# Optimization experiments

Hardware: AMD Instinct MI355X
Metric: run time of the kernel (lower is better)

The kernel has to match this reference:

```python
import jax, jax.numpy as jnp
import numpy as np
from jax import lax

IN_DIM, HID_DIM, OUT_DIM = 1024, 2048, 1024
N_EXP_A, TOPK_A, N_EXP_G = 12, 4, 6
BATCH = 2048
# Shannon entropy (nats) of {1/2, 1/3, 1/6}
H_TARGET = float(-(0.5 * np.log(0.5) + (1.0 / 3.0) * np.log(1.0 / 3.0) + (1.0 / 6.0) * np.log(1.0 / 6.0)))


def setup_inputs() -> dict:
    key = jax.random.key(0)
    ks = jax.random.split(key, 24)
    s_in = 1.0 / np.sqrt(IN_DIM)
    s_hid = 1.0 / np.sqrt(HID_DIM)
    s_out = 1.0 / np.sqrt(OUT_DIM)
    d = {}
    d['x'] = jax.random.normal(ks[0], (BATCH, IN_DIM), dtype=jnp.float32)
    # EngineA: gate + 12 experts (stacked)
    d['gate_a_w'] = jax.random.normal(ks[1], (IN_DIM, N_EXP_A), jnp.float32) * s_in
    d['gate_a_b'] = jnp.zeros((N_EXP_A,), jnp.float32)
    d['wa1'] = jax.random.normal(ks[2], (N_EXP_A, IN_DIM, HID_DIM), jnp.float32) * s_in
    d['ba1'] = jnp.zeros((N_EXP_A, HID_DIM), jnp.float32)
    d['wa2'] = jax.random.normal(ks[3], (N_EXP_A, HID_DIM, OUT_DIM), jnp.float32) * s_hid
    d['ba2'] = jnp.zeros((N_EXP_A, OUT_DIM), jnp.float32)
    # EngineG: gate + 6 experts (stacked)
    d['gate_g_w'] = jax.random.normal(ks[4], (IN_DIM, N_EXP_G), jnp.float32) * s_in
    d['gate_g_b'] = jnp.zeros((N_EXP_G,), jnp.float32)
    d['wg1'] = jax.random.normal(ks[5], (N_EXP_G, IN_DIM, HID_DIM), jnp.float32) * s_in
    d['bg1'] = jnp.zeros((N_EXP_G, HID_DIM), jnp.float32)
    d['wg2'] = jax.random.normal(ks[6], (N_EXP_G, HID_DIM, OUT_DIM), jnp.float32) * s_hid
    d['bg2'] = jnp.zeros((N_EXP_G, OUT_DIM), jnp.float32)
    # self_model: Linear(3,hid) Tanh Linear(hid,out) Tanh
    d['sm_w1'] = jax.random.normal(ks[7], (3, HID_DIM), jnp.float32) * (1.0 / np.sqrt(3.0))
    d['sm_b1'] = jnp.zeros((HID_DIM,), jnp.float32)
    d['sm_w2'] = jax.random.normal(ks[8], (HID_DIM, OUT_DIM), jnp.float32) * s_hid
    d['sm_b2'] = jnp.zeros((OUT_DIM,), jnp.float32)
    # self_influence Linear(out,out)
    d['si_w'] = jax.random.normal(ks[9], (OUT_DIM, OUT_DIM), jnp.float32) * s_out
    d['si_b'] = jnp.zeros((OUT_DIM,), jnp.float32)
    # field_transform Linear(out,out) + Tanh
    d['ft_w'] = jax.random.normal(ks[10], (OUT_DIM, OUT_DIM), jnp.float32) * s_out
    d['ft_b'] = jnp.zeros((OUT_DIM,), jnp.float32)
    d['tension_scale'] = jnp.asarray(1.0 / 3.0, jnp.float32)
    d['n_steps'] = 3
    return d


def _experts(x, w1, b1, w2, b2):
    # x:[B,I], w1:[E,I,H] -> [B,E,O]  (Linear-ReLU-Linear per expert)
    h = jax.nn.relu(jnp.einsum('bi,eih->beh', x, w1) + b1[None])
    return jnp.einsum('beh,eho->beo', h, w2) + b2[None]


def reference(x, gate_a_w, gate_a_b, wa1, ba1, wa2, ba2,
              gate_g_w, gate_g_b, wg1, bg1, wg2, bg2,
              sm_w1, sm_b1, sm_w2, sm_b2, si_w, si_b, ft_w, ft_b,
              tension_scale, n_steps):
    B = x.shape[0]
    # ---- EngineA: top-k (k=4 of 12) MoE ----
    logits_a = x @ gate_a_w + gate_a_b
    topv, topi = lax.top_k(logits_a, TOPK_A)
    topw = jax.nn.softmax(topv, axis=-1)
    weights_a = jnp.zeros_like(logits_a).at[jnp.arange(B)[:, None], topi].set(topw)
    out_a = _experts(x, wa1, ba1, wa2, ba2)            # [B,12,O]
    out_plus = jnp.einsum('be,beo->bo', weights_a, out_a)
    # ---- EngineG: dense-softmax MoE + entropy loss ----
    weights_g = jax.nn.softmax(x @ gate_g_w + gate_g_b, axis=-1)
    out_g = _experts(x, wg1, bg1, wg2, bg2)            # [B,6,O]
    out_minus = jnp.einsum('be,beo->bo', weights_g, out_g)
    h_ent = -(weights_g * jnp.log(weights_g + 1e-8)).sum(-1).mean()
    entropy_loss = (h_ent - H_TARGET) ** 2
    # ---- self-referential loop ----
    repulsion = out_plus - out_minus
    prev_tension = (repulsion ** 2).sum(-1, keepdims=True)      # [B,1]
    tensions = [lax.stop_gradient(prev_tension.mean())]          # .item() detaches
    modified_repulsion = repulsion
    for step in range(n_steps):
        tension_scalar = prev_tension.mean(-1, keepdims=True)    # [B,1]
        if step == 0:
            tension_delta = jnp.zeros_like(tension_scalar)
        else:
            tension_delta = tension_scalar - tensions[-1]
        step_tensor = jnp.full_like(tension_scalar, step / n_steps)
        self_input = jnp.concatenate([tension_scalar, tension_delta, step_tensor], -1)  # [B,3]
        self_state = jnp.tanh(jnp.tanh(self_input @ sm_w1 + sm_b1) @ sm_w2 + sm_b2)
        influence = self_state @ si_w + si_b
        modified_repulsion = repulsion + influence
        prev_tension = (modified_repulsion ** 2).sum(-1, keepdims=True)
        tensions.append(lax.stop_gradient(prev_tension.mean()))
    equilibrium = (out_plus + out_minus) * 0.5
    field_direction = jnp.tanh(modified_repulsion @ ft_w + ft_b)
    output = equilibrium + tension_scale * jnp.sqrt(prev_tension + 1e-8) * field_direction
    t = jnp.stack(tensions)
    convergence_loss = jnp.abs(t[1:] - t[:-1]).mean()            # built from .item()s -> constant
    aux_loss = entropy_loss + 0.001 * convergence_loss
    return output, aux_loss
```

## Files before the change

kernel.cpp:

```cpp
#include <hip/hip_runtime.h>

typedef _Float16 f16;
typedef f16  f16x8 __attribute__((ext_vector_type(8)));
typedef f16  f16x4 __attribute__((ext_vector_type(4)));
typedef float f32x4 __attribute__((ext_vector_type(4)));

#define LOAD_LDS16(gp, lp) __builtin_amdgcn_global_load_lds( \
    (const __attribute__((address_space(1))) void*)(gp),     \
    (__attribute__((address_space(3))) void*)(lp), 16, 0, 0)


__global__ __launch_bounds__(256) void castx_kernel(const float* __restrict__ x,
                                                    f16* __restrict__ o) {
  long i = ((long)blockIdx.x * 256 + threadIdx.x) * 4;
  const float4 v = *(const float4*)(x + i);
  f16x4 h; h.x = (f16)v.x; h.y = (f16)v.y; h.z = (f16)v.z; h.w = (f16)v.w;
  *(f16x4*)(o + i) = h;
}

__global__ __launch_bounds__(256) void transpose_cast(const float* __restrict__ src,
                                                      f16* __restrict__ dst,
                                                      int R, int C, long sbatch,
                                                      long dbatch, int dld) {
  __shared__ float tile[32][33];
  const int zc = blockIdx.x * 32;
  const int zr = blockIdx.y * 32;
  const int z  = blockIdx.z;
  const float* s = src + (long)z * sbatch;
  f16* d = dst + (long)z * dbatch;
  const int tx = threadIdx.x & 31, ty = threadIdx.x >> 5;
#pragma unroll
  for (int rr = 0; rr < 32; rr += 8)
    tile[ty + rr][tx] = s[(long)(zr + ty + rr) * C + (zc + tx)];
  __syncthreads();
#pragma unroll
  for (int rr = 0; rr < 32; rr += 8)
    d[(long)(zc + ty + rr) * dld + (zr + tx)] = (f16)tile[tx][ty + rr];
}

__global__ __launch_bounds__(256) void gating_kernel(
    const float* __restrict__ x, const float* __restrict__ gaw,
    const float* __restrict__ gab, const float* __restrict__ ggw,
    const float* __restrict__ ggb,
    float* __restrict__ wG, float* __restrict__ ent,
    int* __restrict__ rows, float* __restrict__ gval, int* __restrict__ cnt,
    int* __restrict__ eA, int* __restrict__ posA, float* __restrict__ wA4) {
  const int b = blockIdx.x, t = threadIdx.x;
  const float* xr = x + (long)b * 1024;
  float pa[12], pg[6];
#pragma unroll
  for (int e = 0; e < 12; e++) pa[e] = 0.f;
#pragma unroll
  for (int e = 0; e < 6; e++) pg[e] = 0.f;
  const int i0 = t * 4;
  const float4 xv = *(const float4*)(xr + i0);
  const float xs[4] = {xv.x, xv.y, xv.z, xv.w};
#pragma unroll
  for (int u = 0; u < 4; u++) {
    const float xi = xs[u];
    const float* ga = gaw + (long)(i0 + u) * 12;
    const float* gg = ggw + (long)(i0 + u) * 6;
#pragma unroll
    for (int e = 0; e < 12; e++) pa[e] += xi * ga[e];
#pragma unroll
    for (int e = 0; e < 6; e++) pg[e] += xi * gg[e];
  }
#pragma unroll
  for (int e = 0; e < 12; e++)
    for (int m = 1; m < 64; m <<= 1) pa[e] += __shfl_xor(pa[e], m);
#pragma unroll
  for (int e = 0; e < 6; e++)
    for (int m = 1; m < 64; m <<= 1) pg[e] += __shfl_xor(pg[e], m);
  __shared__ float rw[4][18];
  const int lane = t & 63, wv = t >> 6;
  if (lane == 0) {
#pragma unroll
    for (int e = 0; e < 12; e++) rw[wv][e] = pa[e];
#pragma unroll
    for (int e = 0; e < 6; e++) rw[wv][12 + e] = pg[e];
  }
  __syncthreads();
  if (t == 0) {
    float la[12], lg[6];
#pragma unroll
    for (int e = 0; e < 12; e++)
      la[e] = rw[0][e] + rw[1][e] + rw[2][e] + rw[3][e] + gab[e];
#pragma unroll
    for (int e = 0; e < 6; e++)
      lg[e] = rw[0][12 + e] + rw[1][12 + e] + rw[2][12 + e] + rw[3][12 + e] + ggb[e];
    unsigned used = 0; float tv[4]; int tix[4];
    for (int k = 0; k < 4; k++) {
      float best = -3.4e38f; int bi = 0;
      for (int e = 0; e < 12; e++)
        if (!((used >> e) & 1u) && la[e] > best) { best = la[e]; bi = e; }
      tv[k] = best; tix[k] = bi; used |= 1u << bi;
    }
    const float mx = tv[0];
    float s = 0.f, w4[4];
    for (int k = 0; k < 4; k++) { w4[k] = expf(tv[k] - mx); s += w4[k]; }
    for (int k = 0; k < 4; k++) {
      const float w = w4[k] / s;
      const int e = tix[k];
      const int pos = atomicAdd(&cnt[e], 1);
      rows[e * 2048 + pos] = b;
      gval[e * 2048 + pos] = w;
      eA[b * 4 + k] = e;
      posA[b * 4 + k] = pos;
      wA4[b * 4 + k] = w;
    }
    float mg = lg[0];
    for (int e = 1; e < 6; e++) mg = fmaxf(mg, lg[e]);
    float sg = 0.f, wg6[6];
    for (int e = 0; e < 6; e++) { wg6[e] = expf(lg[e] - mg); sg += wg6[e]; }
    float H = 0.f;
    for (int e = 0; e < 6; e++) {
      const float w = wg6[e] / sg;
      wG[b * 6 + e] = w;
      H -= w * logf(w + 1e-8f);
    }
    ent[b] = H;
  }
}

__global__ void base_kernel(const int* __restrict__ cnt, int* __restrict__ baseA) {
  if (threadIdx.x == 0 && blockIdx.x == 0) {
    int r = 0;
    for (int e = 0; e < 12; e++) { baseA[e] = r; r += cnt[e]; }
  }
}

__global__ __launch_bounds__(256) void combine_kernel(
    const f16* __restrict__ res, const int* __restrict__ eA,
    const int* __restrict__ posA, const float* __restrict__ wA4,
    const float* __restrict__ wG, const int* __restrict__ baseA,
    const float* __restrict__ ba2, const float* __restrict__ bg2,
    float* __restrict__ outP, float* __restrict__ outM,
    float* __restrict__ pt0, float* __restrict__ ts0) {
  const long b = blockIdx.x;
  const int t = threadIdx.x;
  const int c = t * 4;
  float4 P = {0.f, 0.f, 0.f, 0.f}, M = {0.f, 0.f, 0.f, 0.f};
#pragma unroll
  for (int k = 0; k < 4; k++) {
    const int e = eA[b * 4 + k];
    const long slot = baseA[e] + posA[b * 4 + k];
    const f16x4 v = *(const f16x4*)(res + slot * 1024 + c);
    const float w = wA4[b * 4 + k];
    const float4 bb = *(const float4*)(ba2 + (long)e * 1024 + c);
    P.x += (float)v.x + w * bb.x; P.y += (float)v.y + w * bb.y;
    P.z += (float)v.z + w * bb.z; P.w += (float)v.w + w * bb.w;
  }
#pragma unroll
  for (int e = 0; e < 6; e++) {
    const f16x4 v = *(const f16x4*)(res + (8192L + e * 2048 + b) * 1024 + c);
    const float w = wG[b * 6 + e];
    const float4 bb = *(const float4*)(bg2 + (long)e * 1024 + c);
    M.x += (float)v.x + w * bb.x; M.y += (float)v.y + w * bb.y;
    M.z += (float)v.z + w * bb.z; M.w += (float)v.w + w * bb.w;
  }
  *(float4*)(outP + b * 1024 + c) = P;
  *(float4*)(outM + b * 1024 + c) = M;
  const float dx = P.x - M.x, dy = P.y - M.y, dz = P.z - M.z, dw = P.w - M.w;
  float s = dx * dx + dy * dy + dz * dz + dw * dw;
#pragma unroll
  for (int m = 1; m < 64; m <<= 1) s += __shfl_xor(s, m);
  __shared__ float rw[4];
  if ((t & 63) == 0) rw[t >> 6] = s;
  __syncthreads();
  if (t == 0) {
    const float tot = rw[0] + rw[1] + rw[2] + rw[3];
    pt0[b] = tot;
    atomicAdd(ts0, tot);
  }
}

__global__ __launch_bounds__(256) void hsm_kernel(
    const float* __restrict__ pt, const float* __restrict__ tsum,
    const float* __restrict__ w1, const float* __restrict__ b1,
    f16* __restrict__ o, int step) {
  const int j = blockIdx.x * 256 + threadIdx.x;
  const int b0 = blockIdx.y * 64;
  const float u0 = w1[j], u1 = w1[2048 + j], u2 = w1[4096 + j], bb = b1[j];
  const float tm = tsum[0] * (1.f / 2048.f);
  const float st = (float)step * (1.f / 3.f);
#pragma unroll 4
  for (int r = 0; r < 64; r++) {
    const int b = b0 + r;
    const float t = pt[b];
    const float delta = (step == 0) ? 0.f : (t - tm);
    o[(long)b * 2048 + j] = (f16)tanhf(t * u0 + delta * u1 + st * u2 + bb);
  }
}

__global__ __launch_bounds__(256) void aux_kernel(const float* __restrict__ ent,
                                                  const float* __restrict__ tsum,
                                                  float* __restrict__ out) {
  const int t = threadIdx.x;
  float s = 0.f;
  for (int i = t; i < 2048; i += 256) s += ent[i];
#pragma unroll
  for (int m = 1; m < 64; m <<= 1) s += __shfl_xor(s, m);
  __shared__ float rw[4];
  if ((t & 63) == 0) rw[t >> 6] = s;
  __syncthreads();
  if (t == 0) {
    const float h = (rw[0] + rw[1] + rw[2] + rw[3]) * (1.f / 2048.f);
    const float d = h - 1.0114042647f;
    const float el = d * d;
    const float t0 = tsum[0] * (1.f / 2048.f), t1 = tsum[1] * (1.f / 2048.f);
    const float t2 = tsum[2] * (1.f / 2048.f), t3 = tsum[3] * (1.f / 2048.f);
    const float conv = (fabsf(t1 - t0) + fabsf(t2 - t1) + fabsf(t3 - t2)) * (1.f / 3.f);
    out[0] = el + 0.001f * conv;
  }
}

__global__ __launch_bounds__(256) void gemm1_kernel(
    const f16* __restrict__ x, const f16* __restrict__ w1t,
    const float* __restrict__ ba1, const float* __restrict__ bg1,
    f16* __restrict__ h, const int* __restrict__ rows,
    const float* __restrict__ gval, const int* __restrict__ cnt,
    const int* __restrict__ baseA, const float* __restrict__ wG) {
  __shared__ f16 Al[2][128 * 32];
  __shared__ f16 Bl[2][128 * 32];
  __shared__ int   Lrow[128];
  __shared__ float Lg[128];
  int id = blockIdx.x;
  int e18, mi, ni, live; long row0; const float* bp;
  if (id < 3072) {
    const int k = id & 7, t = id >> 3;
    mi = t & 15; const int pid = k * 24 + (t >> 4);
    const int e = pid >> 4; ni = pid & 15;
    live = cnt[e] - mi * 128;
    if (live <= 0) return;
    if (live > 128) live = 128;
    row0 = baseA[e] + mi * 128; e18 = e; bp = ba1 + (long)e * 2048;
  } else {
    id -= 3072;
    const int k = id & 7, t = id >> 3;
    mi = t & 15; const int pid = k * 12 + (t >> 4);
    const int e = pid >> 4; ni = pid & 15;
    row0 = 8192L + e * 2048 + mi * 128; live = 128;
    e18 = 12 + e; bp = bg1 + (long)e * 2048;
  }
  const int tid = threadIdx.x;
  const bool routed = (e18 < 12);
  if (tid < 128) {
    const int gi = mi * 128 + tid;
    if (routed) {
      const bool ok = tid < live;
      Lrow[tid] = ok ? rows[e18 * 2048 + gi] : 0;
      Lg[tid]   = ok ? gval[e18 * 2048 + gi] : 0.f;
    } else {
      Lrow[tid] = gi;
      Lg[tid] = wG[gi * 6 + (e18 - 12)];
    }
  }
  __syncthreads();
  const int sc = ((tid & 3) ^ ((tid >> 3) & 3)) * 8;
  const int r0 = Lrow[tid >> 2], r1 = Lrow[64 + (tid >> 2)];
  const f16* a0 = x + (long)r0 * 1024 + sc;
  const f16* a1 = x + (long)r1 * 1024 + sc;
  const f16* b0 = w1t + (long)e18 * 2048 * 1024 + ((long)ni * 128 + (tid >> 2)) * 1024 + sc;
  const f16* b1p = b0 + 64 * 1024;

  const int wave = tid >> 6, lane = tid & 63;
  const int wm = wave & 1, wn = wave >> 1;
  const int l16 = lane & 15, q = lane >> 4;
  const int qa = (q ^ ((l16 >> 1) & 3)) * 8;
  f32x4 acc[4][4] = {};

  LOAD_LDS16(a0, &Al[0][tid * 8]);
  LOAD_LDS16(a1, &Al[0][(256 + tid) * 8]);
  LOAD_LDS16(b0, &Bl[0][tid * 8]);
  LOAD_LDS16(b1p, &Bl[0][(256 + tid) * 8]);
  for (int kk = 0; kk < 32; ++kk) {
    __syncthreads();
    const int cur = kk & 1;
    if (kk + 1 < 32) {
      const long k0 = (long)(kk + 1) * 32;
      const int nb = cur ^ 1;
      LOAD_LDS16(a0 + k0, &Al[nb][tid * 8]);
      LOAD_LDS16(a1 + k0, &Al[nb][(256 + tid) * 8]);
      LOAD_LDS16(b0 + k0, &Bl[nb][tid * 8]);
      LOAD_LDS16(b1p + k0, &Bl[nb][(256 + tid) * 8]);
    }
    f16x8 av[4], bv[4];
#pragma unroll
    for (int i = 0; i < 4; i++)
      av[i] = *(const f16x8*)&Al[cur][(wm * 64 + i * 16 + l16) * 32 + qa];
#pragma unroll
    for (int j = 0; j < 4; j++)
      bv[j] = *(const f16x8*)&Bl[cur][(wn * 64 + j * 16 + l16) * 32 + qa];
#pragma unroll
    for (int i = 0; i < 4; i++)
#pragma unroll
      for (int j = 0; j < 4; j++)
        acc[i][j] = __builtin_amdgcn_mfma_f32_16x16x32_f16(av[i], bv[j], acc[i][j], 0, 0, 0);
  }
#pragma unroll
  for (int i = 0; i < 4; i++) {
#pragma unroll
    for (int r = 0; r < 4; r++) {
      const int lr = wm * 64 + i * 16 + q * 4 + r;
      if (lr < live) {
        const float wv = Lg[lr];
        f16* C = h + (row0 + lr) * 2048;
#pragma unroll
        for (int j = 0; j < 4; j++) {
          const int gc = ni * 128 + wn * 64 + j * 16 + l16;
          const float v = fmaxf(acc[i][j][r] + bp[gc], 0.f) * wv;
          C[gc] = (f16)v;
        }
      }
    }
  }
}

__global__ __launch_bounds__(256) void gemm2_kernel(
    const f16* __restrict__ h, const f16* __restrict__ w2t,
    f16* __restrict__ res, const int* __restrict__ cnt,
    const int* __restrict__ baseA) {
  __shared__ f16 Al[2][128 * 32];
  __shared__ f16 Bl[2][128 * 32];
  int id = blockIdx.x;
  int e18, mi, ni, live; long row0;
  if (id < 1536) {
    const int k = id & 7, t = id >> 3;
    mi = t & 15; const int pid = k * 12 + (t >> 4);
    const int e = pid >> 3; ni = pid & 7;
    live = cnt[e] - mi * 128;
    if (live <= 0) return;
    if (live > 128) live = 128;
    row0 = baseA[e] + mi * 128; e18 = e;
  } else {
    id -= 1536;
    const int k = id & 7, t = id >> 3;
    mi = t & 15; const int pid = k * 6 + (t >> 4);
    const int e = pid >> 3; ni = pid & 7;
    row0 = 8192L + e * 2048 + mi * 128; live = 128; e18 = 12 + e;
  }
  const int tid = threadIdx.x;
  const int sc = ((tid & 3) ^ ((tid >> 3) & 3)) * 8;
  const f16* a0 = h + (row0 + (tid >> 2)) * 2048 + sc;
  const f16* a1 = a0 + 64 * 2048;
  const f16* b0 = w2t + (long)e18 * 1024 * 2048 + ((long)ni * 128 + (tid >> 2)) * 2048 + sc;
  const f16* b1p = b0 + 64 * 2048;

  const int wave = tid >> 6, lane = tid & 63;
  const int wm = wave & 1, wn = wave >> 1;
  const int l16 = lane & 15, q = lane >> 4;
  const int qa = (q ^ ((l16 >> 1) & 3)) * 8;
  f32x4 acc[4][4] = {};

  LOAD_LDS16(a0, &Al[0][tid * 8]);
  LOAD_LDS16(a1, &Al[0][(256 + tid) * 8]);
  LOAD_LDS16(b0, &Bl[0][tid * 8]);
  LOAD_LDS16(b1p, &Bl[0][(256 + tid) * 8]);
  for (int kk = 0; kk < 64; ++kk) {
    __syncthreads();
    const int cur = kk & 1;
    if (kk + 1 < 64) {
      const long k0 = (long)(kk + 1) * 32;
      const int nb = cur ^ 1;
      LOAD_LDS16(a0 + k0, &Al[nb][tid * 8]);
      LOAD_LDS16(a1 + k0, &Al[nb][(256 + tid) * 8]);
      LOAD_LDS16(b0 + k0, &Bl[nb][tid * 8]);
      LOAD_LDS16(b1p + k0, &Bl[nb][(256 + tid) * 8]);
    }
    f16x8 av[4], bv[4];
#pragma unroll
    for (int i = 0; i < 4; i++)
      av[i] = *(const f16x8*)&Al[cur][(wm * 64 + i * 16 + l16) * 32 + qa];
#pragma unroll
    for (int j = 0; j < 4; j++)
      bv[j] = *(const f16x8*)&Bl[cur][(wn * 64 + j * 16 + l16) * 32 + qa];
#pragma unroll
    for (int i = 0; i < 4; i++)
#pragma unroll
      for (int j = 0; j < 4; j++)
        acc[i][j] = __builtin_amdgcn_mfma_f32_16x16x32_f16(av[i], bv[j], acc[i][j], 0, 0, 0);
  }
#pragma unroll
  for (int i = 0; i < 4; i++) {
#pragma unroll
    for (int r = 0; r < 4; r++) {
      const int lr = wm * 64 + i * 16 + q * 4 + r;
      if (lr < live) {
        f16* C = res + (row0 + lr) * 1024 + ni * 128;
#pragma unroll
        for (int j = 0; j < 4; j++) {
          const int gc = wn * 64 + j * 16 + l16;
          C[gc] = (f16)acc[i][j][r];
        }
      }
    }
  }
}


struct GA {
  const f16* A; long lda;
  const f16* B; long ldb;
  int nk;
  float* Cf; f16* Ch;
  const float* bias;
  const float* op; const float* om;
  const float* pt; const float* ts;
  float* pt_out; float* tsum_out;
};

template <int EPI>
__global__ __launch_bounds__(256) void gemm_s(GA a) {
  __shared__ f16 Al[2][64 * 32];
  __shared__ f16 Bl[2][64 * 32];
  const int tid = threadIdx.x;
  const int wave = tid >> 6, lane = tid & 63;
  const int wm = wave & 1, wn = wave >> 1;
  const int l16 = lane & 15, q = lane >> 4;
  const int qa = (q ^ ((l16 >> 1) & 3)) * 8;
  const long m0 = (long)blockIdx.y * 64;
  const long n0 = (long)blockIdx.x * 64;
  const int sc = ((tid & 3) ^ ((tid >> 3) & 3)) * 8;
  const f16* a0 = a.A + (m0 + (tid >> 2)) * a.lda + sc;
  const f16* b0 = a.B + (n0 + (tid >> 2)) * a.ldb + sc;
  f32x4 acc[2][2] = {};
  LOAD_LDS16(a0, &Al[0][tid * 8]);
  LOAD_LDS16(b0, &Bl[0][tid * 8]);
  for (int kk = 0; kk < a.nk; ++kk) {
    __syncthreads();
    const int cur = kk & 1;
    if (kk + 1 < a.nk) {
      const long k0 = (long)(kk + 1) * 32;
      const int nb = cur ^ 1;
      LOAD_LDS16(a0 + k0, &Al[nb][tid * 8]);
      LOAD_LDS16(b0 + k0, &Bl[nb][tid * 8]);
    }
    f16x8 av[2], bv[2];
#pragma unroll
    for (int i = 0; i < 2; i++)
      av[i] = *(const f16x8*)&Al[cur][(wm * 32 + i * 16 + l16) * 32 + qa];
#pragma unroll
    for (int j = 0; j < 2; j++)
      bv[j] = *(const f16x8*)&Bl[cur][(wn * 32 + j * 16 + l16) * 32 + qa];
#pragma unroll
    for (int i = 0; i < 2; i++)
#pragma unroll
      for (int j = 0; j < 2; j++)
        acc[i][j] = __builtin_amdgcn_mfma_f32_16x16x32_f16(av[i], bv[j], acc[i][j], 0, 0, 0);
  }
  if constexpr (EPI == 2) {
#pragma unroll
    for (int i = 0; i < 2; i++)
#pragma unroll
      for (int r = 0; r < 4; r++) {
        const long gr = m0 + wm * 32 + i * 16 + q * 4 + r;
#pragma unroll
        for (int j = 0; j < 2; j++) {
          const int gc = (int)n0 + wn * 32 + j * 16 + l16;
          a.Ch[gr * 1024 + gc] = (f16)tanhf(acc[i][j][r] + a.bias[gc]);
        }
      }
  } else if constexpr (EPI == 3) {
    float wave_ss = 0.f;
#pragma unroll
    for (int i = 0; i < 2; i++)
#pragma unroll
      for (int r = 0; r < 4; r++) {
        const long gr = m0 + wm * 32 + i * 16 + q * 4 + r;
        float ss = 0.f;
#pragma unroll
        for (int j = 0; j < 2; j++) {
          const int gc = (int)n0 + wn * 32 + j * 16 + l16;
          const long ix = gr * 1024 + gc;
          const float v = (a.op[ix] - a.om[ix]) + acc[i][j][r] + a.bias[gc];
          a.Ch[ix] = (f16)v;
          ss += v * v;
        }
        ss += __shfl_xor(ss, 1); ss += __shfl_xor(ss, 2);
        ss += __shfl_xor(ss, 4); ss += __shfl_xor(ss, 8);
        if (l16 == 0) {
          atomicAdd(a.pt_out + gr, ss);
          wave_ss += ss;
        }
      }
    wave_ss += __shfl_xor(wave_ss, 16);
    wave_ss += __shfl_xor(wave_ss, 32);
    if (lane == 0) atomicAdd(a.tsum_out, wave_ss);
  } else {
    const float tsc = a.ts[0];
#pragma unroll
    for (int i = 0; i < 2; i++)
#pragma unroll
      for (int r = 0; r < 4; r++) {
        const long gr = m0 + wm * 32 + i * 16 + q * 4 + r;
        const float sq = sqrtf(a.pt[gr] + 1e-8f) * tsc;
#pragma unroll
        for (int j = 0; j < 2; j++) {
          const int gc = (int)n0 + wn * 32 + j * 16 + l16;
          const long ix = gr * 1024 + gc;
          const float v = tanhf(acc[i][j][r] + a.bias[gc]);
          a.Cf[ix] = 0.5f * (a.op[ix] + a.om[ix]) + sq * v;
        }
      }
  }
}


extern "C" void kernel_launch(void* const* d_in, const int* in_sizes, int n_in,
                              void* d_out, int out_size, void* d_ws, size_t ws_size,
                              hipStream_t stream) {
  (void)in_sizes; (void)n_in; (void)out_size; (void)ws_size;
  const float* x    = (const float*)d_in[0];
  const float* gaw  = (const float*)d_in[1];
  const float* gab  = (const float*)d_in[2];
  const float* wa1  = (const float*)d_in[3];
  const float* ba1  = (const float*)d_in[4];
  const float* wa2  = (const float*)d_in[5];
  const float* ba2  = (const float*)d_in[6];
  const float* ggw  = (const float*)d_in[7];
  const float* ggb  = (const float*)d_in[8];
  const float* wg1  = (const float*)d_in[9];
  const float* bg1  = (const float*)d_in[10];
  const float* wg2  = (const float*)d_in[11];
  const float* bg2  = (const float*)d_in[12];
  const float* smw1 = (const float*)d_in[13];
  const float* smb1 = (const float*)d_in[14];
  const float* smw2 = (const float*)d_in[15];
  const float* smb2 = (const float*)d_in[16];
  const float* siw  = (const float*)d_in[17];
  const float* sib  = (const float*)d_in[18];
  const float* ftw  = (const float*)d_in[19];
  const float* ftb  = (const float*)d_in[20];
  const float* tsc  = (const float*)d_in[21];

  char* p = (char*)d_ws;
  size_t off = 0;
  auto alloc = [&](size_t bytes) -> char* {
    char* r = p + off;
    off = (off + bytes + 255) & ~(size_t)255;
    return r;
  };
  f16* xb     = (f16*)alloc(2048UL * 1024 * 2);
  f16* w1t    = (f16*)alloc(18UL * 2048 * 1024 * 2);
  f16* smw2t  = (f16*)alloc(1024UL * 2048 * 2);
  f16* sit    = (f16*)alloc(1024UL * 1024 * 2);
  f16* ftt    = (f16*)alloc(1024UL * 1024 * 2);
  f16* h      = (f16*)alloc(20480UL * 2048 * 2);
  f16* res    = (f16*)alloc(20480UL * 1024 * 2);
  float* outP = (float*)alloc(2048UL * 1024 * 4);
  float* outM = (float*)alloc(2048UL * 1024 * 4);
  f16* hsmb   = (f16*)alloc(2048UL * 2048 * 2);
  f16* sst    = (f16*)alloc(2048UL * 1024 * 2);
  f16* modb   = (f16*)alloc(2048UL * 1024 * 2);
  float* entb = (float*)alloc(2048 * 4);
  float* wGb  = (float*)alloc(2048 * 6 * 4);
  float* ptb  = (float*)alloc(4 * 2048 * 4);
  float* tsb  = (float*)alloc(4 * 4);
  int*   cntb = (int*)alloc(12 * 4);
  int*   baseAb = (int*)alloc(12 * 4);
  int*   rowsb  = (int*)alloc(12 * 2048 * 4);
  float* gvalb  = (float*)alloc(12 * 2048 * 4);
  int*   eAb    = (int*)alloc(2048 * 4 * 4);
  int*   posAb  = (int*)alloc(2048 * 4 * 4);
  float* wA4b   = (float*)alloc(2048 * 4 * 4);

  f16* w2t = w1t;

  hipMemsetAsync(ptb, 0, 33072, stream);

  transpose_cast<<<dim3(64, 32, 12), 256, 0, stream>>>(wa1, w1t, 1024, 2048,
      1024L * 2048, 2048L * 1024, 1024);
  transpose_cast<<<dim3(64, 32, 6), 256, 0, stream>>>(wg1, w1t + 12UL * 2048 * 1024,
      1024, 2048, 1024L * 2048, 2048L * 1024, 1024);
  transpose_cast<<<dim3(32, 64, 1), 256, 0, stream>>>(smw2, smw2t, 2048, 1024, 0, 0, 2048);
  transpose_cast<<<dim3(32, 32, 1), 256, 0, stream>>>(siw, sit, 1024, 1024, 0, 0, 1024);
  transpose_cast<<<dim3(32, 32, 1), 256, 0, stream>>>(ftw, ftt, 1024, 1024, 0, 0, 1024);
  castx_kernel<<<2048, 256, 0, stream>>>(x, xb);
  gating_kernel<<<2048, 256, 0, stream>>>(x, gaw, gab, ggw, ggb, wGb, entb,
                                          rowsb, gvalb, cntb, eAb, posAb, wA4b);
  base_kernel<<<1, 64, 0, stream>>>(cntb, baseAb);

  gemm1_kernel<<<4608, 256, 0, stream>>>(xb, w1t, ba1, bg1, h,
                                         rowsb, gvalb, cntb, baseAb, wGb);

  transpose_cast<<<dim3(32, 64, 12), 256, 0, stream>>>(wa2, w2t, 2048, 1024,
      2048L * 1024, 1024L * 2048, 2048);
  transpose_cast<<<dim3(32, 64, 6), 256, 0, stream>>>(wg2, w2t + 12UL * 1024 * 2048,
      2048, 1024, 2048L * 1024, 1024L * 2048, 2048);

  gemm2_kernel<<<2304, 256, 0, stream>>>(h, w2t, res, cntb, baseAb);

  combine_kernel<<<2048, 256, 0, stream>>>(res, eAb, posAb, wA4b, wGb, baseAb,
                                           ba2, bg2, outP, outM, ptb, tsb);

  for (int s = 0; s < 3; s++) {
    hsm_kernel<<<dim3(8, 32), 256, 0, stream>>>(ptb + s * 2048, tsb + s, smw1, smb1, hsmb, s);
    GA g3{};
    g3.A = hsmb; g3.lda = 2048; g3.B = smw2t; g3.ldb = 2048; g3.nk = 64;
    g3.Ch = sst; g3.bias = smb2;
    gemm_s<2><<<dim3(16, 32), 256, 0, stream>>>(g3);
    GA g4{};
    g4.A = sst; g4.lda = 1024; g4.B = sit; g4.ldb = 1024; g4.nk = 32;
    g4.Ch = modb; g4.bias = sib; g4.op = outP; g4.om = outM;
    g4.pt_out = ptb + (s + 1) * 2048; g4.tsum_out = tsb + (s + 1);
    gemm_s<3><<<dim3(16, 32), 256, 0, stream>>>(g4);
  }

  GA g5{};
  g5.A = modb; g5.lda = 1024; g5.B = ftt; g5.ldb = 1024; g5.nk = 32;
  g5.Cf = (float*)d_out; g5.bias = ftb; g5.op = outP; g5.om = outM;
  g5.pt = ptb + 3 * 2048; g5.ts = tsc;
  gemm_s<4><<<dim3(16, 32), 256, 0, stream>>>(g5);

  aux_kernel<<<1, 256, 0, stream>>>(entb, tsb, (float*)d_out + 2048UL * 1024);
}
```

Baseline: 1.042 ms.

## Merge small launches and deepen gemm_s K-tile to 64

Merges the paired expert-weight transposes into one launch each and combines the three small-weight transposes into a single multi-descriptor kernel. The x-to-f16 cast moves into the gating kernel, and the aux-loss reduction moves into the final GEMM's epilogue, which drops several kernel launches. The small GEMM now uses a 64-wide K tile with a new XOR swizzle, halving its loop iterations and barriers at the cost of twice the LDS per block. The merged transpose3 grid launches some blocks that exit early, and the fused aux reduction adds a barrier to block (0,0) only.

```diff
diff --git a/kernel.cpp b/kernel.cpp
--- a/kernel.cpp
+++ b/kernel.cpp
@@ -10,23 +10,17 @@
     (__attribute__((address_space(3))) void*)(lp), 16, 0, 0)
 
 
-__global__ __launch_bounds__(256) void castx_kernel(const float* __restrict__ x,
-                                                    f16* __restrict__ o) {
-  long i = ((long)blockIdx.x * 256 + threadIdx.x) * 4;
-  const float4 v = *(const float4*)(x + i);
-  f16x4 h; h.x = (f16)v.x; h.y = (f16)v.y; h.z = (f16)v.z; h.w = (f16)v.w;
-  *(f16x4*)(o + i) = h;
-}
-
-__global__ __launch_bounds__(256) void transpose_cast(const float* __restrict__ src,
-                                                      f16* __restrict__ dst,
-                                                      int R, int C, long sbatch,
-                                                      long dbatch, int dld) {
+__global__ __launch_bounds__(256) void transpose_cast2(const float* __restrict__ s0,
+                                                       const float* __restrict__ s1,
+                                                       int zsplit, f16* __restrict__ dst,
+                                                       int R, int C, long sbatch,
+                                                       long dbatch, int dld) {
   __shared__ float tile[32][33];
   const int zc = blockIdx.x * 32;
   const int zr = blockIdx.y * 32;
   const int z  = blockIdx.z;
-  const float* s = src + (long)z * sbatch;
+  const float* s = (z < zsplit) ? (s0 + (long)z * sbatch)
+                                : (s1 + (long)(z - zsplit) * sbatch);
   f16* d = dst + (long)z * dbatch;
   const int tx = threadIdx.x & 31, ty = threadIdx.x >> 5;
 #pragma unroll
@@ -38,10 +32,29 @@
     d[(long)(zc + ty + rr) * dld + (zr + tx)] = (f16)tile[tx][ty + rr];
 }
 
+struct TDesc { const float* s; f16* d; int R; int C; int dld; };
+struct TDesc3 { TDesc m[3]; };
+
+__global__ __launch_bounds__(256) void transpose3(TDesc3 p) {
+  const TDesc t = p.m[blockIdx.z];
+  const int zc = blockIdx.x * 32;
+  const int zr = blockIdx.y * 32;
+  if (zr >= t.R || zc >= t.C) return;
+  __shared__ float tile[32][33];
+  const int tx = threadIdx.x & 31, ty = threadIdx.x >> 5;
+#pragma unroll
+  for (int rr = 0; rr < 32; rr += 8)
+    tile[ty + rr][tx] = t.s[(long)(zr + ty + rr) * t.C + (zc + tx)];
+  __syncthreads();
+#pragma unroll
+  for (int rr = 0; rr < 32; rr += 8)
+    t.d[(long)(zc + ty + rr) * t.dld + (zr + tx)] = (f16)tile[tx][ty + rr];
+}
+
 __global__ __launch_bounds__(256) void gating_kernel(
     const float* __restrict__ x, const float* __restrict__ gaw,
     const float* __restrict__ gab, const float* __restrict__ ggw,
-    const float* __restrict__ ggb,
+    const float* __restrict__ ggb, f16* __restrict__ xb,
     float* __restrict__ wG, float* __restrict__ ent,
     int* __restrict__ rows, float* __restrict__ gval, int* __restrict__ cnt,
     int* __restrict__ eA, int* __restrict__ posA, float* __restrict__ wA4) {
@@ -54,6 +67,8 @@
   for (int e = 0; e < 6; e++) pg[e] = 0.f;
   const int i0 = t * 4;
   const float4 xv = *(const float4*)(xr + i0);
+  f16x4 hx; hx.x = (f16)xv.x; hx.y = (f16)xv.y; hx.z = (f16)xv.z; hx.w = (f16)xv.w;
+  *(f16x4*)(xb + (long)b * 1024 + i0) = hx;
   const float xs[4] = {xv.x, xv.y, xv.z, xv.w};
 #pragma unroll
   for (int u = 0; u < 4; u++) {
@@ -189,28 +204,6 @@
     const float t = pt[b];
     const float delta = (step == 0) ? 0.f : (t - tm);
     o[(long)b * 2048 + j] = (f16)tanhf(t * u0 + delta * u1 + st * u2 + bb);
-  }
-}
-
-__global__ __launch_bounds__(256) void aux_kernel(const float* __restrict__ ent,
-                                                  const float* __restrict__ tsum,
-                                                  float* __restrict__ out) {
-  const int t = threadIdx.x;
-  float s = 0.f;
-  for (int i = t; i < 2048; i += 256) s += ent[i];
-#pragma unroll
-  for (int m = 1; m < 64; m <<= 1) s += __shfl_xor(s, m);
-  __shared__ float rw[4];
-  if ((t & 63) == 0) rw[t >> 6] = s;
-  __syncthreads();
-  if (t == 0) {
-    const float h = (rw[0] + rw[1] + rw[2] + rw[3]) * (1.f / 2048.f);
-    const float d = h - 1.0114042647f;
-    const float el = d * d;
-    const float t0 = tsum[0] * (1.f / 2048.f), t1 = tsum[1] * (1.f / 2048.f);
-    const float t2 = tsum[2] * (1.f / 2048.f), t3 = tsum[3] * (1.f / 2048.f);
-    const float conv = (fabsf(t1 - t0) + fabsf(t2 - t1) + fabsf(t3 - t2)) * (1.f / 3.f);
-    out[0] = el + 0.001f * conv;
   }
 }
 
@@ -407,46 +400,60 @@
   const float* op; const float* om;
   const float* pt; const float* ts;
   float* pt_out; float* tsum_out;
+  const float* ent; const float* tsb; float* aux_out;
 };
 
 template <int EPI>
 __global__ __launch_bounds__(256) void gemm_s(GA a) {
-  __shared__ f16 Al[2][64 * 32];
-  __shared__ f16 Bl[2][64 * 32];
+  __shared__ f16 Al[2][64 * 64];
+  __shared__ f16 Bl[2][64 * 64];
   const int tid = threadIdx.x;
   const int wave = tid >> 6, lane = tid & 63;
   const int wm = wave & 1, wn = wave >> 1;
   const int l16 = lane & 15, q = lane >> 4;
-  const int qa = (q ^ ((l16 >> 1) & 3)) * 8;
   const long m0 = (long)blockIdx.y * 64;
   const long n0 = (long)blockIdx.x * 64;
-  const int sc = ((tid & 3) ^ ((tid >> 3) & 3)) * 8;
-  const f16* a0 = a.A + (m0 + (tid >> 2)) * a.lda + sc;
-  const f16* b0 = a.B + (n0 + (tid >> 2)) * a.ldb + sc;
+  const int srow = tid >> 3;
+  const int sch  = ((tid & 7) ^ (srow & 7)) * 8;
+  const f16* a0 = a.A + (m0 + srow) * a.lda + sch;
+  const f16* a1 = a.A + (m0 + srow + 32) * a.lda + sch;
+  const f16* b0 = a.B + (n0 + srow) * a.ldb + sch;
+  const f16* b1 = a.B + (n0 + srow + 32) * a.ldb + sch;
+  const int rx = (l16 & 7) * 8;
   f32x4 acc[2][2] = {};
   LOAD_LDS16(a0, &Al[0][tid * 8]);
+  LOAD_LDS16(a1, &Al[0][(256 + tid) * 8]);
   LOAD_LDS16(b0, &Bl[0][tid * 8]);
+  LOAD_LDS16(b1, &Bl[0][(256 + tid) * 8]);
   for (int kk = 0; kk < a.nk; ++kk) {
     __syncthreads();
     const int cur = kk & 1;
     if (kk + 1 < a.nk) {
-      const long k0 = (long)(kk + 1) * 32;
+      const long k0 = (long)(kk + 1) * 64;
       const int nb = cur ^ 1;
       LOAD_LDS16(a0 + k0, &Al[nb][tid * 8]);
+      LOAD_LDS16(a1 + k0, &Al[nb][(256 + tid) * 8]);
       LOAD_LDS16(b0 + k0, &Bl[nb][tid * 8]);
-    }
-    f16x8 av[2], bv[2];
-#pragma unroll
-    for (int i = 0; i < 2; i++)
-      av[i] = *(const f16x8*)&Al[cur][(wm * 32 + i * 16 + l16) * 32 + qa];
-#pragma unroll
-    for (int j = 0; j < 2; j++)
-      bv[j] = *(const f16x8*)&Bl[cur][(wn * 32 + j * 16 + l16) * 32 + qa];
-#pragma unroll
-    for (int i = 0; i < 2; i++)
+      LOAD_LDS16(b1 + k0, &Bl[nb][(256 + tid) * 8]);
+    }
+    f16x8 av[2][2], bv[2][2];
+#pragma unroll
+    for (int hf = 0; hf < 2; hf++) {
+      const int cA = (((hf * 4 + q) * 8) ^ rx);
+#pragma unroll
+      for (int i = 0; i < 2; i++)
+        av[hf][i] = *(const f16x8*)&Al[cur][(wm * 32 + i * 16 + l16) * 64 + cA];
 #pragma unroll
       for (int j = 0; j < 2; j++)
-        acc[i][j] = __builtin_amdgcn_mfma_f32_16x16x32_f16(av[i], bv[j], acc[i][j], 0, 0, 0);
+        bv[hf][j] = *(const f16x8*)&Bl[cur][(wn * 32 + j * 16 + l16) * 64 + cA];
+    }
+#pragma unroll
+    for (int hf = 0; hf < 2; hf++)
+#pragma unroll
+      for (int i = 0; i < 2; i++)
+#pragma unroll
+        for (int j = 0; j < 2; j++)
+          acc[i][j] = __builtin_amdgcn_mfma_f32_16x16x32_f16(av[hf][i], bv[hf][j], acc[i][j], 0, 0, 0);
   }
   if constexpr (EPI == 2) {
 #pragma unroll
@@ -502,6 +509,24 @@
           a.Cf[ix] = 0.5f * (a.op[ix] + a.om[ix]) + sq * v;
         }
       }
+    if (blockIdx.x == 0 && blockIdx.y == 0) {
+      float s = 0.f;
+      for (int i = tid; i < 2048; i += 256) s += a.ent[i];
+#pragma unroll
+      for (int m = 1; m < 64; m <<= 1) s += __shfl_xor(s, m);
+      __shared__ float rwa[4];
+      if ((tid & 63) == 0) rwa[tid >> 6] = s;
+      __syncthreads();
+      if (tid == 0) {
+        const float hh = (rwa[0] + rwa[1] + rwa[2] + rwa[3]) * (1.f / 2048.f);
+        const float dd = hh - 1.0114042647f;
+        const float el = dd * dd;
+        const float t0 = a.tsb[0] * (1.f / 2048.f), t1 = a.tsb[1] * (1.f / 2048.f);
+        const float t2 = a.tsb[2] * (1.f / 2048.f), t3 = a.tsb[3] * (1.f / 2048.f);
+        const float conv = (fabsf(t1 - t0) + fabsf(t2 - t1) + fabsf(t3 - t2)) * (1.f / 3.f);
+        a.aux_out[0] = el + 0.001f * conv;
+      }
+    }
   }
 }
 
@@ -568,24 +593,23 @@
 
   hipMemsetAsync(ptb, 0, 33072, stream);
 
-  transpose_cast<<<dim3(64, 32, 12), 256, 0, stream>>>(wa1, w1t, 1024, 2048,
-      1024L * 2048, 2048L * 1024, 1024);
-  transpose_cast<<<dim3(64, 32, 6), 256, 0, stream>>>(wg1, w1t + 12UL * 2048 * 1024,
+  transpose_cast2<<<dim3(64, 32, 18), 256, 0, stream>>>(wa1, wg1, 12, w1t,
       1024, 2048, 1024L * 2048, 2048L * 1024, 1024);
-  transpose_cast<<<dim3(32, 64, 1), 256, 0, stream>>>(smw2, smw2t, 2048, 1024, 0, 0, 2048);
-  transpose_cast<<<dim3(32, 32, 1), 256, 0, stream>>>(siw, sit, 1024, 1024, 0, 0, 1024);
-  transpose_cast<<<dim3(32, 32, 1), 256, 0, stream>>>(ftw, ftt, 1024, 1024, 0, 0, 1024);
-  castx_kernel<<<2048, 256, 0, stream>>>(x, xb);
-  gating_kernel<<<2048, 256, 0, stream>>>(x, gaw, gab, ggw, ggb, wGb, entb,
+  {
+    TDesc3 td;
+    td.m[0] = {smw2, smw2t, 2048, 1024, 2048};
+    td.m[1] = {siw,  sit,  1024, 1024, 1024};
+    td.m[2] = {ftw,  ftt,  1024, 1024, 1024};
+    transpose3<<<dim3(32, 64, 3), 256, 0, stream>>>(td);
+  }
+  gating_kernel<<<2048, 256, 0, stream>>>(x, gaw, gab, ggw, ggb, xb, wGb, entb,
                                           rowsb, gvalb, cntb, eAb, posAb, wA4b);
   base_kernel<<<1, 64, 0, stream>>>(cntb, baseAb);
 
   gemm1_kernel<<<4608, 256, 0, stream>>>(xb, w1t, ba1, bg1, h,
                                          rowsb, gvalb, cntb, baseAb, wGb);
 
-  transpose_cast<<<dim3(32, 64, 12), 256, 0, stream>>>(wa2, w2t, 2048, 1024,
-      2048L * 1024, 1024L * 2048, 2048);
-  transpose_cast<<<dim3(32, 64, 6), 256, 0, stream>>>(wg2, w2t + 12UL * 1024 * 2048,
+  transpose_cast2<<<dim3(32, 64, 18), 256, 0, stream>>>(wa2, wg2, 12, w2t,
       2048, 1024, 2048L * 1024, 1024L * 2048, 2048);
 
   gemm2_kernel<<<2304, 256, 0, stream>>>(h, w2t, res, cntb, baseAb);
@@ -596,21 +620,20 @@
   for (int s = 0; s < 3; s++) {
     hsm_kernel<<<dim3(8, 32), 256, 0, stream>>>(ptb + s * 2048, tsb + s, smw1, smb1, hsmb, s);
     GA g3{};
-    g3.A = hsmb; g3.lda = 2048; g3.B = smw2t; g3.ldb = 2048; g3.nk = 64;
+    g3.A = hsmb; g3.lda = 2048; g3.B = smw2t; g3.ldb = 2048; g3.nk = 32;
     g3.Ch = sst; g3.bias = smb2;
     gemm_s<2><<<dim3(16, 32), 256, 0, stream>>>(g3);
     GA g4{};
-    g4.A = sst; g4.lda = 1024; g4.B = sit; g4.ldb = 1024; g4.nk = 32;
+    g4.A = sst; g4.lda = 1024; g4.B = sit; g4.ldb = 1024; g4.nk = 16;
     g4.Ch = modb; g4.bias = sib; g4.op = outP; g4.om = outM;
     g4.pt_out = ptb + (s + 1) * 2048; g4.tsum_out = tsb + (s + 1);
     gemm_s<3><<<dim3(16, 32), 256, 0, stream>>>(g4);
   }
 
   GA g5{};
-  g5.A = modb; g5.lda = 1024; g5.B = ftt; g5.ldb = 1024; g5.nk = 32;
+  g5.A = modb; g5.lda = 1024; g5.B = ftt; g5.ldb = 1024; g5.nk = 16;
   g5.Cf = (float*)d_out; g5.bias = ftb; g5.op = outP; g5.om = outM;
   g5.pt = ptb + 3 * 2048; g5.ts = tsc;
+  g5.ent = entb; g5.tsb = tsb; g5.aux_out = (float*)d_out + 2048UL * 1024;
   gemm_s<4><<<dim3(16, 32), 256, 0, stream>>>(g5);
-
-  aux_kernel<<<1, 256, 0, stream>>>(entb, tsb, (float*)d_out + 2048UL * 1024);
-}
+}
```

Result: faster. 1.016 ms (-2.5%).
